# Kernel optimization log

Measured on AMD Instinct MI355X. Metric: run time of the kernel, lower is better.

## Reference

```python
import jax, jax.numpy as jnp
import numpy as np

B, S_NEW, D = 8, 16, 2048
H, HD = 16, 128
PAST = 4096


def setup_inputs() -> dict:
    key = jax.random.key(0)
    ks = jax.random.split(key, 8)
    w = 0.02
    return {
        "x": jax.random.normal(ks[0], (B, S_NEW, D), jnp.float32),
        "k_cache": jax.random.normal(ks[1], (B, H, PAST, HD), jnp.float32),
        "v_cache": jax.random.normal(ks[2], (B, H, PAST, HD), jnp.float32),
        "Wq": jax.random.normal(ks[3], (D, D), jnp.float32) * w,
        "bq": jnp.zeros((D,), jnp.float32),
        "Wk": jax.random.normal(ks[4], (D, D), jnp.float32) * w,
        "bk": jnp.zeros((D,), jnp.float32),
        "Wv": jax.random.normal(ks[5], (D, D), jnp.float32) * w,
        "bv": jnp.zeros((D,), jnp.float32),
        "Wo": jax.random.normal(ks[6], (D, D), jnp.float32) * w,
        "bo": jnp.zeros((D,), jnp.float32),
    }


def reference(x, k_cache, v_cache, Wq, bq, Wk, bk, Wv, bv, Wo, bo):
    B_, S_new, D_ = x.shape
    H_ = H
    hd = D_ // H_
    scale = hd ** (-0.5)

    def proj(W, b):
        # [B,S,D] -> [B,H,S,hd]
        return (x @ W + b).reshape(B_, S_new, H_, hd).transpose(0, 2, 1, 3)

    q = proj(Wq, bq)
    k_new = proj(Wk, bk)
    v_new = proj(Wv, bv)

    # cache.append + get_full_kv: concat along sequence axis
    k = jnp.concatenate([k_cache, k_new], axis=2)  # [B,H,S_full,hd]
    v = jnp.concatenate([v_cache, v_new], axis=2)
    S_full = k.shape[2]
    past = S_full - S_new

    scores = jnp.einsum("bhqd,bhkd->bhqk", q, k) * scale  # [B,H,S_new,S_full]

    # triu(ones(S_new,S_full), diagonal=past+1): mask key j when j - i > past
    i = jnp.arange(S_new)[:, None]
    j = jnp.arange(S_full)[None, :]
    mask = (j - i) > past  # [S_new, S_full] bool
    scores = jnp.where(mask[None, None, :, :], -jnp.inf, scores)

    attn = jax.nn.softmax(scores, axis=-1)  # dropout is identity in eval
    out = jnp.einsum("bhqk,bhkd->bhqd", attn, v)  # [B,H,S_new,hd]
    out = out.transpose(0, 2, 1, 3).reshape(B_, S_new, D_)
    return out @ Wo + bo
```

## Files before the change

### kernel.cpp

```cpp
#include <hip/hip_runtime.h>
#include <stdint.h>

#define B_    8
#define SNEW  16
#define D_    2048
#define H_    16
#define HD_   128
#define PAST_ 4096
#define SCALE 0.08838834764831845f

#define NCHUNK 16

typedef __attribute__((ext_vector_type(8))) short bf16x8;
typedef __attribute__((ext_vector_type(4))) float f32x4;

union BF8 { bf16x8 v; unsigned int u[4]; unsigned short s[8]; };

__device__ __forceinline__ unsigned short f2bf(float f) {
  union { float f; unsigned int u; } c; c.f = f;
  unsigned int r = c.u + 0x7fffu + ((c.u >> 16) & 1u);
  return (unsigned short)(r >> 16);
}
__device__ __forceinline__ unsigned int pk2(float a, float b) {
  return (unsigned int)f2bf(a) | ((unsigned int)f2bf(b) << 16);
}

__global__ __launch_bounds__(256) void k_cvt_x(const float* __restrict__ x,
                                               unsigned short* __restrict__ xb) {
  int i = blockIdx.x * 256 + threadIdx.x;
  const float4* xs = (const float4*)x;
  float4 a = xs[i * 2], b = xs[i * 2 + 1];
  uint4 v;
  v.x = pk2(a.x, a.y); v.y = pk2(a.z, a.w);
  v.z = pk2(b.x, b.y); v.w = pk2(b.z, b.w);
  ((uint4*)xb)[i] = v;
}

__global__ __launch_bounds__(256) void k_qkv(
    const unsigned short* __restrict__ xb,
    const float* __restrict__ Wq, const float* __restrict__ bq,
    const float* __restrict__ Wk, const float* __restrict__ bk,
    const float* __restrict__ Wv, const float* __restrict__ bv,
    unsigned short* __restrict__ qb, unsigned short* __restrict__ kbn,
    unsigned short* __restrict__ vbn) {
  __shared__ float red[4][128][16];
  const int n0g = blockIdx.x * 16;
  const int mat = n0g >> 11;
  const int n0 = n0g & 2047;
  const float* W    = (mat == 0) ? Wq : ((mat == 1) ? Wk : Wv);
  const float* bias = (mat == 0) ? bq : ((mat == 1) ? bk : bv);
  const int tid = threadIdx.x, w = tid >> 6, lane = tid & 63;
  const int nl = lane & 15, g = lane >> 4;

  f32x4 acc[8];
#pragma unroll
  for (int i = 0; i < 8; i++) acc[i] = (f32x4){0.f, 0.f, 0.f, 0.f};

  const int k0w = w * 512;
  for (int kc = 0; kc < 16; kc++) {
    const int kbase = k0w + kc * 32 + g * 8;
    float bw[8];
#pragma unroll
    for (int j = 0; j < 8; j++) bw[j] = W[(size_t)(kbase + j) * 2048 + n0 + nl];
    BF8 bf;
#pragma unroll
    for (int j2 = 0; j2 < 4; j2++) bf.u[j2] = pk2(bw[2 * j2], bw[2 * j2 + 1]);
#pragma unroll
    for (int mt = 0; mt < 8; mt++) {
      bf16x8 a = *(const bf16x8*)(xb + (size_t)(mt * 16 + nl) * 2048 + kbase);
      acc[mt] = __builtin_amdgcn_mfma_f32_16x16x32_bf16(a, bf.v, acc[mt], 0, 0, 0);
    }
  }
#pragma unroll
  for (int mt = 0; mt < 8; mt++) {
    red[w][mt * 16 + g * 4 + 0][nl] = acc[mt][0];
    red[w][mt * 16 + g * 4 + 1][nl] = acc[mt][1];
    red[w][mt * 16 + g * 4 + 2][nl] = acc[mt][2];
    red[w][mt * 16 + g * 4 + 3][nl] = acc[mt][3];
  }
  __syncthreads();
  const int m = tid >> 1;
  const int c0 = (tid & 1) * 8;
  float sv[8];
#pragma unroll
  for (int i = 0; i < 8; i++)
    sv[i] = red[0][m][c0 + i] + red[1][m][c0 + i] + red[2][m][c0 + i] +
            red[3][m][c0 + i] + bias[n0 + c0 + i];
  const int bb = m >> 4, srow = m & 15;
  const int nglob = n0 + c0;
  const int hh = nglob >> 7, dd = nglob & 127;
  size_t ob = (((size_t)(bb * H_ + hh) * SNEW + srow) * HD_ + dd);
  uint4 v;
  if (mat == 0) {
    v.x = pk2(sv[0] * SCALE, sv[1] * SCALE); v.y = pk2(sv[2] * SCALE, sv[3] * SCALE);
    v.z = pk2(sv[4] * SCALE, sv[5] * SCALE); v.w = pk2(sv[6] * SCALE, sv[7] * SCALE);
    *(uint4*)(qb + ob) = v;
  } else {
    v.x = pk2(sv[0], sv[1]); v.y = pk2(sv[2], sv[3]);
    v.z = pk2(sv[4], sv[5]); v.w = pk2(sv[6], sv[7]);
    if (mat == 1) *(uint4*)(kbn + ob) = v;
    else          *(uint4*)(vbn + ob) = v;
  }
}

__global__ __launch_bounds__(256) void k_attn(
    const float* __restrict__ kcache, const float* __restrict__ vcache,
    const unsigned short* __restrict__ qb, const unsigned short* __restrict__ kbn,
    const unsigned short* __restrict__ vbn,
    float* __restrict__ pO, float* __restrict__ pml) {
  __shared__ char smem[17408 * 2 + 4352 + 5120];
  unsigned short* Klds = (unsigned short*)smem;
  unsigned short* Vlds = (unsigned short*)(smem + 17408);
  unsigned short* Qlds = (unsigned short*)(smem + 34816);
  unsigned short* Plds = (unsigned short*)(smem + 34816 + 4352);
  float* cO  = (float*)smem;
  float* cml = (float*)(smem + 32768);

  const int chunk = blockIdx.x;
  const int h = blockIdx.y, b = blockIdx.z;
  const int bh = b * H_ + h;
  const int tid = threadIdx.x;
  const int w = tid >> 6, lane = tid & 63;
  const int nl = lane & 15, g = lane >> 4;

  {
    uint4 v = ((const uint4*)(qb + (size_t)bh * 2048))[tid];
    int e = tid * 8;
    *(uint4*)(Qlds + (e >> 7) * 136 + (e & 127)) = v;
  }
  for (int i = tid; i < 1280; i += 256) ((unsigned int*)Plds)[i] = 0u;
  __syncthreads();

  bf16x8 qfrag[4];
#pragma unroll
  for (int kc4 = 0; kc4 < 4; kc4++)
    qfrag[kc4] = *(const bf16x8*)(Qlds + nl * 136 + kc4 * 32 + g * 8);

  unsigned short* Kw = Klds + w * (16 * 136);
  unsigned short* Vw = Vlds + w * (16 * 136);
  unsigned short* Pw = Plds + w * (16 * 40);

  f32x4 Oacc[8];
#pragma unroll
  for (int i = 0; i < 8; i++) Oacc[i] = (f32x4){0.f, 0.f, 0.f, 0.f};
  float m_run = -1e30f, l_run = 0.f;

  const int CK = PAST_ / NCHUNK;
  const int key0 = chunk * CK + w * (CK / 4);
  const int NIT = CK / 4 / 16;
  const bool lastw = (chunk == NCHUNK - 1) && (w == 3);
  const int itend = NIT + (lastw ? 1 : 0);

  for (int it = 0; it < itend; it++) {
    if (it < NIT) {
      const float4* ks = (const float4*)(kcache + ((size_t)bh * PAST_ + key0 + it * 16) * HD_);
      const float4* vs = (const float4*)(vcache + ((size_t)bh * PAST_ + key0 + it * 16) * HD_);
#pragma unroll
      for (int i = 0; i < 8; i++) {
        float4 kv = ks[lane + i * 64];
        int e = (lane + i * 64) * 4;
        uint2 p; p.x = pk2(kv.x, kv.y); p.y = pk2(kv.z, kv.w);
        *(uint2*)(Kw + (e >> 7) * 136 + (e & 127)) = p;
      }
#pragma unroll
      for (int i = 0; i < 8; i++) {
        float4 vv = vs[lane + i * 64];
        int e = (lane + i * 64) * 4;
        uint2 p; p.x = pk2(vv.x, vv.y); p.y = pk2(vv.z, vv.w);
        *(uint2*)(Vw + (e >> 7) * 136 + (e & 127)) = p;
      }
    } else {
      const uint4* ks = (const uint4*)(kbn + (size_t)bh * 2048);
      const uint4* vs = (const uint4*)(vbn + (size_t)bh * 2048);
#pragma unroll
      for (int i = 0; i < 4; i++) {
        uint4 v = ks[lane + i * 64];
        int e = (lane + i * 64) * 8;
        *(uint4*)(Kw + (e >> 7) * 136 + (e & 127)) = v;
        uint4 v2 = vs[lane + i * 64];
        *(uint4*)(Vw + (e >> 7) * 136 + (e & 127)) = v2;
      }
    }

    f32x4 sacc = (f32x4){0.f, 0.f, 0.f, 0.f};
#pragma unroll
    for (int kc4 = 0; kc4 < 4; kc4++) {
      bf16x8 a = *(const bf16x8*)(Kw + nl * 136 + kc4 * 32 + g * 8);
      sacc = __builtin_amdgcn_mfma_f32_16x16x32_bf16(a, qfrag[kc4], sacc, 0, 0, 0);
    }
    float s0 = sacc[0], s1 = sacc[1], s2 = sacc[2], s3 = sacc[3];
    if (it == NIT) {
      if (g * 4 + 0 > nl) s0 = -1e30f;
      if (g * 4 + 1 > nl) s1 = -1e30f;
      if (g * 4 + 2 > nl) s2 = -1e30f;
      if (g * 4 + 3 > nl) s3 = -1e30f;
    }
    float kmax = fmaxf(fmaxf(s0, s1), fmaxf(s2, s3));
    kmax = fmaxf(kmax, __shfl_xor(kmax, 16, 64));
    kmax = fmaxf(kmax, __shfl_xor(kmax, 32, 64));
    float newm = fmaxf(m_run, kmax);
    float p0 = __expf(s0 - newm), p1 = __expf(s1 - newm);
    float p2 = __expf(s2 - newm), p3 = __expf(s3 - newm);
    float psum = p0 + p1 + p2 + p3;
    psum += __shfl_xor(psum, 16, 64);
    psum += __shfl_xor(psum, 32, 64);
    float alpha = __expf(m_run - newm);
    l_run = l_run * alpha + psum;
    m_run = newm;
    float ar0 = __shfl(alpha, g * 4 + 0, 64);
    float ar1 = __shfl(alpha, g * 4 + 1, 64);
    float ar2 = __shfl(alpha, g * 4 + 2, 64);
    float ar3 = __shfl(alpha, g * 4 + 3, 64);
#pragma unroll
    for (int nt = 0; nt < 8; nt++) {
      Oacc[nt][0] *= ar0; Oacc[nt][1] *= ar1;
      Oacc[nt][2] *= ar2; Oacc[nt][3] *= ar3;
    }
    *(unsigned int*)(Pw + nl * 40 + g * 4)     = pk2(p0, p1);
    *(unsigned int*)(Pw + nl * 40 + g * 4 + 2) = pk2(p2, p3);
    bf16x8 pfrag = *(const bf16x8*)(Pw + nl * 40 + g * 8);
#pragma unroll
    for (int nt = 0; nt < 8; nt++) {
      BF8 vb;
#pragma unroll
      for (int j2 = 0; j2 < 4; j2++) {
        int ka = (g * 8 + j2 * 2) & 15;
        int kb2 = (g * 8 + j2 * 2 + 1) & 15;
        unsigned int lo = Vw[ka * 136 + nt * 16 + nl];
        unsigned int hi = Vw[kb2 * 136 + nt * 16 + nl];
        vb.u[j2] = lo | (hi << 16);
      }
      Oacc[nt] = __builtin_amdgcn_mfma_f32_16x16x32_bf16(pfrag, vb.v, Oacc[nt], 0, 0, 0);
    }
  }

  __syncthreads();
  float* cOw = cO + w * (16 * 128);
#pragma unroll
  for (int nt = 0; nt < 8; nt++) {
    cOw[(g * 4 + 0) * 128 + nt * 16 + nl] = Oacc[nt][0];
    cOw[(g * 4 + 1) * 128 + nt * 16 + nl] = Oacc[nt][1];
    cOw[(g * 4 + 2) * 128 + nt * 16 + nl] = Oacc[nt][2];
    cOw[(g * 4 + 3) * 128 + nt * 16 + nl] = Oacc[nt][3];
  }
  if (g == 0) { cml[(w * 16 + nl) * 2] = m_run; cml[(w * 16 + nl) * 2 + 1] = l_run; }
  __syncthreads();

  const int q = tid >> 4;
  const int d0 = (tid & 15) * 8;
  float M = -1e30f, mws[4], lws[4];
#pragma unroll
  for (int ww = 0; ww < 4; ww++) {
    mws[ww] = cml[(ww * 16 + q) * 2];
    lws[ww] = cml[(ww * 16 + q) * 2 + 1];
    M = fmaxf(M, mws[ww]);
  }
  float L = 0.f, o[8];
#pragma unroll
  for (int i = 0; i < 8; i++) o[i] = 0.f;
#pragma unroll
  for (int ww = 0; ww < 4; ww++) {
    float Wt = __expf(mws[ww] - M);
    L += Wt * lws[ww];
    const float* src = cO + ww * 2048 + q * 128 + d0;
#pragma unroll
    for (int i = 0; i < 8; i++) o[i] += Wt * src[i];
  }
  size_t pb = (((size_t)bh * NCHUNK + chunk) * 16 + q) * 128 + d0;
  float4 st0 = {o[0], o[1], o[2], o[3]}, st1 = {o[4], o[5], o[6], o[7]};
  *(float4*)(pO + pb) = st0;
  *(float4*)(pO + pb + 4) = st1;
  if ((tid & 15) == 0) {
    size_t mb = (((size_t)bh * NCHUNK + chunk) * 16 + q) * 2;
    pml[mb] = M; pml[mb + 1] = L;
  }
}

__global__ __launch_bounds__(256) void k_comb(const float* __restrict__ pO,
                                              const float* __restrict__ pml,
                                              float* __restrict__ attn) {
  const int bh = blockIdx.x, tid = threadIdx.x;
  const int q = tid >> 4, d0 = (tid & 15) * 8;
  float M = -1e30f, mc[NCHUNK], lc[NCHUNK];
#pragma unroll
  for (int c = 0; c < NCHUNK; c++) {
    size_t mb = (((size_t)bh * NCHUNK + c) * 16 + q) * 2;
    mc[c] = pml[mb]; lc[c] = pml[mb + 1];
    M = fmaxf(M, mc[c]);
  }
  float L = 0.f, o[8];
#pragma unroll
  for (int i = 0; i < 8; i++) o[i] = 0.f;
#pragma unroll
  for (int c = 0; c < NCHUNK; c++) {
    float Wt = __expf(mc[c] - M);
    L += Wt * lc[c];
    const float* src = pO + (((size_t)bh * NCHUNK + c) * 16 + q) * 128 + d0;
#pragma unroll
    for (int i = 0; i < 8; i++) o[i] += Wt * src[i];
  }
  float inv = 1.f / L;
  int b = bh >> 4, h = bh & 15;
  float* dst = attn + ((size_t)(b * SNEW + q)) * D_ + h * HD_ + d0;
  float4 s0 = {o[0] * inv, o[1] * inv, o[2] * inv, o[3] * inv};
  float4 s1 = {o[4] * inv, o[5] * inv, o[6] * inv, o[7] * inv};
  *(float4*)dst = s0;
  *(float4*)(dst + 4) = s1;
}

__global__ __launch_bounds__(256) void k_oproj(const float* __restrict__ attn,
                                               const float* __restrict__ Wo,
                                               const float* __restrict__ bo,
                                               float* __restrict__ out) {
  __shared__ float red[4][128][16];
  const int n0 = blockIdx.x * 16;
  const int tid = threadIdx.x, w = tid >> 6, lane = tid & 63;
  const int nl = lane & 15, g = lane >> 4;
  f32x4 acc[8];
#pragma unroll
  for (int i = 0; i < 8; i++) acc[i] = (f32x4){0.f, 0.f, 0.f, 0.f};
  const int k0w = w * 512;
  for (int kc = 0; kc < 16; kc++) {
    const int kbase = k0w + kc * 32 + g * 8;
    float bw[8];
#pragma unroll
    for (int j = 0; j < 8; j++) bw[j] = Wo[(size_t)(kbase + j) * 2048 + n0 + nl];
    BF8 bf;
#pragma unroll
    for (int j2 = 0; j2 < 4; j2++) bf.u[j2] = pk2(bw[2 * j2], bw[2 * j2 + 1]);
#pragma unroll
    for (int mt = 0; mt < 8; mt++) {
      const float* ap = attn + (size_t)(mt * 16 + nl) * 2048 + kbase;
      float4 a0 = *(const float4*)ap;
      float4 a1 = *(const float4*)(ap + 4);
      BF8 af;
      af.u[0] = pk2(a0.x, a0.y); af.u[1] = pk2(a0.z, a0.w);
      af.u[2] = pk2(a1.x, a1.y); af.u[3] = pk2(a1.z, a1.w);
      acc[mt] = __builtin_amdgcn_mfma_f32_16x16x32_bf16(af.v, bf.v, acc[mt], 0, 0, 0);
    }
  }
#pragma unroll
  for (int mt = 0; mt < 8; mt++) {
    red[w][mt * 16 + g * 4 + 0][nl] = acc[mt][0];
    red[w][mt * 16 + g * 4 + 1][nl] = acc[mt][1];
    red[w][mt * 16 + g * 4 + 2][nl] = acc[mt][2];
    red[w][mt * 16 + g * 4 + 3][nl] = acc[mt][3];
  }
  __syncthreads();
  const int m = tid >> 1;
  const int c0 = (tid & 1) * 8;
  float sv[8];
#pragma unroll
  for (int i = 0; i < 8; i++)
    sv[i] = red[0][m][c0 + i] + red[1][m][c0 + i] + red[2][m][c0 + i] +
            red[3][m][c0 + i] + bo[n0 + c0 + i];
  float* dst = out + (size_t)m * 2048 + n0 + c0;
  float4 s0 = {sv[0], sv[1], sv[2], sv[3]}, s1 = {sv[4], sv[5], sv[6], sv[7]};
  *(float4*)dst = s0;
  *(float4*)(dst + 4) = s1;
}

extern "C" void kernel_launch(void* const* d_in, const int* in_sizes, int n_in,
                              void* d_out, int out_size, void* d_ws, size_t ws_size,
                              hipStream_t stream) {
  const float* x  = (const float*)d_in[0];
  const float* kc = (const float*)d_in[1];
  const float* vc = (const float*)d_in[2];
  const float* Wq = (const float*)d_in[3];
  const float* bq = (const float*)d_in[4];
  const float* Wk = (const float*)d_in[5];
  const float* bk = (const float*)d_in[6];
  const float* Wv = (const float*)d_in[7];
  const float* bv = (const float*)d_in[8];
  const float* Wo = (const float*)d_in[9];
  const float* bo = (const float*)d_in[10];
  float* out = (float*)d_out;

  char* ws = (char*)d_ws;
  unsigned short* xb   = (unsigned short*)(ws + 0);
  unsigned short* qb   = (unsigned short*)(ws + 524288);
  unsigned short* kbn  = (unsigned short*)(ws + 1048576);
  unsigned short* vbn  = (unsigned short*)(ws + 1572864);
  float*          attn = (float*)(ws + 2097152);
  float*          pO   = (float*)(ws + 3145728);
  float*          pml  = (float*)(ws + 19922944);

  k_cvt_x<<<128, 256, 0, stream>>>(x, xb);
  k_qkv<<<384, 256, 0, stream>>>(xb, Wq, bq, Wk, bk, Wv, bv, qb, kbn, vbn);
  k_attn<<<dim3(NCHUNK, H_, B_), 256, 0, stream>>>(kc, vc, qb, kbn, vbn, pO, pml);
  k_comb<<<B_ * H_, 256, 0, stream>>>(pO, pml, attn);
  k_oproj<<<128, 256, 0, stream>>>(attn, Wo, bo, out);
}
```

Before: 661.4 us.

## Prefetch K/V and weights into registers, transpose V in LDS, use exp2 softmax

The attention kernel now register-prefetches the next K/V cache tile while the current one is processed. V is stored transposed in LDS with an XOR swizzle so the PV MFMA operand loads become four dword reads instead of sixteen scattered shorts. Q is pre-scaled by log2(e) so the softmax can use exp2, and bf16 packing uses the hardware v_cvt_pk_bf16_f32 instruction. The projection GEMMs software-pipeline their weight loads one k-step ahead, and launch bounds request 3 blocks per SM, which adds register pressure and possible spills.

```diff
diff --git a/kernel.cpp b/kernel.cpp
--- a/kernel.cpp
+++ b/kernel.cpp
@@ -7,22 +7,24 @@
 #define H_    16
 #define HD_   128
 #define PAST_ 4096
+#define LOG2E 1.4426950408889634f
 #define SCALE 0.08838834764831845f
+#define QSCALE (SCALE * LOG2E)
 
 #define NCHUNK 16
+
+#define KSTRIDE 136
+#define VSTRIDE 18
 
 typedef __attribute__((ext_vector_type(8))) short bf16x8;
 typedef __attribute__((ext_vector_type(4))) float f32x4;
 
 union BF8 { bf16x8 v; unsigned int u[4]; unsigned short s[8]; };
 
-__device__ __forceinline__ unsigned short f2bf(float f) {
-  union { float f; unsigned int u; } c; c.f = f;
-  unsigned int r = c.u + 0x7fffu + ((c.u >> 16) & 1u);
-  return (unsigned short)(r >> 16);
-}
 __device__ __forceinline__ unsigned int pk2(float a, float b) {
-  return (unsigned int)f2bf(a) | ((unsigned int)f2bf(b) << 16);
+  unsigned int r;
+  asm("v_cvt_pk_bf16_f32 %0, %1, %2" : "=v"(r) : "v"(a), "v"(b));
+  return r;
 }
 
 __global__ __launch_bounds__(256) void k_cvt_x(const float* __restrict__ x,
@@ -57,11 +59,17 @@
   for (int i = 0; i < 8; i++) acc[i] = (f32x4){0.f, 0.f, 0.f, 0.f};
 
   const int k0w = w * 512;
+  float bw[8];
+#pragma unroll
+  for (int j = 0; j < 8; j++) bw[j] = W[(size_t)(k0w + g * 8 + j) * 2048 + n0 + nl];
+
   for (int kc = 0; kc < 16; kc++) {
     const int kbase = k0w + kc * 32 + g * 8;
-    float bw[8];
-#pragma unroll
-    for (int j = 0; j < 8; j++) bw[j] = W[(size_t)(kbase + j) * 2048 + n0 + nl];
+    float nbw[8];
+    if (kc < 15) {
+#pragma unroll
+      for (int j = 0; j < 8; j++) nbw[j] = W[(size_t)(kbase + 32 + j) * 2048 + n0 + nl];
+    }
     BF8 bf;
 #pragma unroll
     for (int j2 = 0; j2 < 4; j2++) bf.u[j2] = pk2(bw[2 * j2], bw[2 * j2 + 1]);
@@ -69,6 +77,10 @@
     for (int mt = 0; mt < 8; mt++) {
       bf16x8 a = *(const bf16x8*)(xb + (size_t)(mt * 16 + nl) * 2048 + kbase);
       acc[mt] = __builtin_amdgcn_mfma_f32_16x16x32_bf16(a, bf.v, acc[mt], 0, 0, 0);
+    }
+    if (kc < 15) {
+#pragma unroll
+      for (int j = 0; j < 8; j++) bw[j] = nbw[j];
     }
   }
 #pragma unroll
@@ -92,8 +104,8 @@
   size_t ob = (((size_t)(bb * H_ + hh) * SNEW + srow) * HD_ + dd);
   uint4 v;
   if (mat == 0) {
-    v.x = pk2(sv[0] * SCALE, sv[1] * SCALE); v.y = pk2(sv[2] * SCALE, sv[3] * SCALE);
-    v.z = pk2(sv[4] * SCALE, sv[5] * SCALE); v.w = pk2(sv[6] * SCALE, sv[7] * SCALE);
+    v.x = pk2(sv[0] * QSCALE, sv[1] * QSCALE); v.y = pk2(sv[2] * QSCALE, sv[3] * QSCALE);
+    v.z = pk2(sv[4] * QSCALE, sv[5] * QSCALE); v.w = pk2(sv[6] * QSCALE, sv[7] * QSCALE);
     *(uint4*)(qb + ob) = v;
   } else {
     v.x = pk2(sv[0], sv[1]); v.y = pk2(sv[2], sv[3]);
@@ -103,16 +115,15 @@
   }
 }
 
-__global__ __launch_bounds__(256) void k_attn(
+__global__ __launch_bounds__(256, 3) void k_attn(
     const float* __restrict__ kcache, const float* __restrict__ vcache,
     const unsigned short* __restrict__ qb, const unsigned short* __restrict__ kbn,
     const unsigned short* __restrict__ vbn,
     float* __restrict__ pO, float* __restrict__ pml) {
-  __shared__ char smem[17408 * 2 + 4352 + 5120];
+  __shared__ char smem[40960];
   unsigned short* Klds = (unsigned short*)smem;
   unsigned short* Vlds = (unsigned short*)(smem + 17408);
-  unsigned short* Qlds = (unsigned short*)(smem + 34816);
-  unsigned short* Plds = (unsigned short*)(smem + 34816 + 4352);
+  unsigned short* QP   = (unsigned short*)(smem + 35840);
   float* cO  = (float*)smem;
   float* cml = (float*)(smem + 32768);
 
@@ -123,51 +134,74 @@
   const int w = tid >> 6, lane = tid & 63;
   const int nl = lane & 15, g = lane >> 4;
 
-  {
-    uint4 v = ((const uint4*)(qb + (size_t)bh * 2048))[tid];
-    int e = tid * 8;
-    *(uint4*)(Qlds + (e >> 7) * 136 + (e & 127)) = v;
-  }
-  for (int i = tid; i < 1280; i += 256) ((unsigned int*)Plds)[i] = 0u;
-  __syncthreads();
-
-  bf16x8 qfrag[4];
-#pragma unroll
-  for (int kc4 = 0; kc4 < 4; kc4++)
-    qfrag[kc4] = *(const bf16x8*)(Qlds + nl * 136 + kc4 * 32 + g * 8);
-
-  unsigned short* Kw = Klds + w * (16 * 136);
-  unsigned short* Vw = Vlds + w * (16 * 136);
-  unsigned short* Pw = Plds + w * (16 * 40);
-
-  f32x4 Oacc[8];
-#pragma unroll
-  for (int i = 0; i < 8; i++) Oacc[i] = (f32x4){0.f, 0.f, 0.f, 0.f};
-  float m_run = -1e30f, l_run = 0.f;
-
   const int CK = PAST_ / NCHUNK;
   const int key0 = chunk * CK + w * (CK / 4);
   const int NIT = CK / 4 / 16;
   const bool lastw = (chunk == NCHUNK - 1) && (w == 3);
   const int itend = NIT + (lastw ? 1 : 0);
 
+  const float4* kbase = (const float4*)(kcache + ((size_t)bh * PAST_ + key0) * HD_);
+  const float4* vbase = (const float4*)(vcache + ((size_t)bh * PAST_ + key0) * HD_);
+
+  float4 kreg[8], vreg[8];
+#pragma unroll
+  for (int i = 0; i < 8; i++) kreg[i] = kbase[lane + i * 64];
+#pragma unroll
+  for (int i = 0; i < 8; i++) vreg[i] = vbase[lane + i * 64];
+
+  {
+    uint4 v = ((const uint4*)(qb + (size_t)bh * 2048))[tid];
+    int e = tid * 8;
+    *(uint4*)(QP + (e >> 7) * KSTRIDE + (e & 127)) = v;
+  }
+  __syncthreads();
+  bf16x8 qfrag[4];
+#pragma unroll
+  for (int kc4 = 0; kc4 < 4; kc4++)
+    qfrag[kc4] = *(const bf16x8*)(QP + nl * KSTRIDE + kc4 * 32 + g * 8);
+  __syncthreads();
+  for (int i = tid; i < 1280; i += 256) ((unsigned int*)QP)[i] = 0u;
+  __syncthreads();
+
+  unsigned short* Kw = Klds + w * (16 * KSTRIDE);
+  unsigned short* Vw = Vlds + w * (128 * VSTRIDE);
+  unsigned short* Pw = QP + w * (16 * 40);
+
+  f32x4 Oacc[8];
+#pragma unroll
+  for (int i = 0; i < 8; i++) Oacc[i] = (f32x4){0.f, 0.f, 0.f, 0.f};
+  float m_run = -1e30f, l_run = 0.f;
+
   for (int it = 0; it < itend; it++) {
     if (it < NIT) {
-      const float4* ks = (const float4*)(kcache + ((size_t)bh * PAST_ + key0 + it * 16) * HD_);
-      const float4* vs = (const float4*)(vcache + ((size_t)bh * PAST_ + key0 + it * 16) * HD_);
 #pragma unroll
       for (int i = 0; i < 8; i++) {
-        float4 kv = ks[lane + i * 64];
+        float4 kv = kreg[i];
         int e = (lane + i * 64) * 4;
         uint2 p; p.x = pk2(kv.x, kv.y); p.y = pk2(kv.z, kv.w);
-        *(uint2*)(Kw + (e >> 7) * 136 + (e & 127)) = p;
+        *(uint2*)(Kw + (e >> 7) * KSTRIDE + (e & 127)) = p;
       }
 #pragma unroll
       for (int i = 0; i < 8; i++) {
-        float4 vv = vs[lane + i * 64];
-        int e = (lane + i * 64) * 4;
-        uint2 p; p.x = pk2(vv.x, vv.y); p.y = pk2(vv.z, vv.w);
-        *(uint2*)(Vw + (e >> 7) * 136 + (e & 127)) = p;
+        float4 vv = vreg[i];
+        int idx = lane + i * 64;
+        int r = idx >> 5;
+        int d0 = (idx & 31) * 4;
+        unsigned int c01 = pk2(vv.x, vv.y);
+        unsigned int c23 = pk2(vv.z, vv.w);
+        int rs = r ^ (((d0 >> 5) & 1) << 3);
+        Vw[(d0 + 0) * VSTRIDE + rs] = (unsigned short)c01;
+        Vw[(d0 + 1) * VSTRIDE + rs] = (unsigned short)(c01 >> 16);
+        Vw[(d0 + 2) * VSTRIDE + rs] = (unsigned short)c23;
+        Vw[(d0 + 3) * VSTRIDE + rs] = (unsigned short)(c23 >> 16);
+      }
+      if (it + 1 < NIT) {
+        const float4* kn = kbase + (size_t)(it + 1) * 512;
+        const float4* vn = vbase + (size_t)(it + 1) * 512;
+#pragma unroll
+        for (int i = 0; i < 8; i++) kreg[i] = kn[lane + i * 64];
+#pragma unroll
+        for (int i = 0; i < 8; i++) vreg[i] = vn[lane + i * 64];
       }
     } else {
       const uint4* ks = (const uint4*)(kbn + (size_t)bh * 2048);
@@ -176,16 +210,28 @@
       for (int i = 0; i < 4; i++) {
         uint4 v = ks[lane + i * 64];
         int e = (lane + i * 64) * 8;
-        *(uint4*)(Kw + (e >> 7) * 136 + (e & 127)) = v;
+        *(uint4*)(Kw + (e >> 7) * KSTRIDE + (e & 127)) = v;
+      }
+#pragma unroll
+      for (int i = 0; i < 4; i++) {
         uint4 v2 = vs[lane + i * 64];
-        *(uint4*)(Vw + (e >> 7) * 136 + (e & 127)) = v2;
+        int idx = lane + i * 64;
+        int r = idx >> 4;
+        int d0 = (idx & 15) * 8;
+        int rs = r ^ (((d0 >> 5) & 1) << 3);
+        unsigned int uu[4] = {v2.x, v2.y, v2.z, v2.w};
+#pragma unroll
+        for (int j2 = 0; j2 < 4; j2++) {
+          Vw[(d0 + 2 * j2 + 0) * VSTRIDE + rs] = (unsigned short)uu[j2];
+          Vw[(d0 + 2 * j2 + 1) * VSTRIDE + rs] = (unsigned short)(uu[j2] >> 16);
+        }
       }
     }
 
     f32x4 sacc = (f32x4){0.f, 0.f, 0.f, 0.f};
 #pragma unroll
     for (int kc4 = 0; kc4 < 4; kc4++) {
-      bf16x8 a = *(const bf16x8*)(Kw + nl * 136 + kc4 * 32 + g * 8);
+      bf16x8 a = *(const bf16x8*)(Kw + nl * KSTRIDE + kc4 * 32 + g * 8);
       sacc = __builtin_amdgcn_mfma_f32_16x16x32_bf16(a, qfrag[kc4], sacc, 0, 0, 0);
     }
     float s0 = sacc[0], s1 = sacc[1], s2 = sacc[2], s3 = sacc[3];
@@ -199,12 +245,12 @@
     kmax = fmaxf(kmax, __shfl_xor(kmax, 16, 64));
     kmax = fmaxf(kmax, __shfl_xor(kmax, 32, 64));
     float newm = fmaxf(m_run, kmax);
-    float p0 = __expf(s0 - newm), p1 = __expf(s1 - newm);
-    float p2 = __expf(s2 - newm), p3 = __expf(s3 - newm);
+    float p0 = exp2f(s0 - newm), p1 = exp2f(s1 - newm);
+    float p2 = exp2f(s2 - newm), p3 = exp2f(s3 - newm);
     float psum = p0 + p1 + p2 + p3;
     psum += __shfl_xor(psum, 16, 64);
     psum += __shfl_xor(psum, 32, 64);
-    float alpha = __expf(m_run - newm);
+    float alpha = exp2f(m_run - newm);
     l_run = l_run * alpha + psum;
     m_run = newm;
     float ar0 = __shfl(alpha, g * 4 + 0, 64);
@@ -221,15 +267,11 @@
     bf16x8 pfrag = *(const bf16x8*)(Pw + nl * 40 + g * 8);
 #pragma unroll
     for (int nt = 0; nt < 8; nt++) {
+      int row = nt * 16 + nl;
+      const unsigned int* vp = (const unsigned int*)(
+          Vw + row * VSTRIDE + (((g & 1) << 3) ^ ((nt & 2) << 2)));
       BF8 vb;
-#pragma unroll
-      for (int j2 = 0; j2 < 4; j2++) {
-        int ka = (g * 8 + j2 * 2) & 15;
-        int kb2 = (g * 8 + j2 * 2 + 1) & 15;
-        unsigned int lo = Vw[ka * 136 + nt * 16 + nl];
-        unsigned int hi = Vw[kb2 * 136 + nt * 16 + nl];
-        vb.u[j2] = lo | (hi << 16);
-      }
+      vb.u[0] = vp[0]; vb.u[1] = vp[1]; vb.u[2] = vp[2]; vb.u[3] = vp[3];
       Oacc[nt] = __builtin_amdgcn_mfma_f32_16x16x32_bf16(pfrag, vb.v, Oacc[nt], 0, 0, 0);
     }
   }
@@ -260,7 +302,7 @@
   for (int i = 0; i < 8; i++) o[i] = 0.f;
 #pragma unroll
   for (int ww = 0; ww < 4; ww++) {
-    float Wt = __expf(mws[ww] - M);
+    float Wt = exp2f(mws[ww] - M);
     L += Wt * lws[ww];
     const float* src = cO + ww * 2048 + q * 128 + d0;
 #pragma unroll
@@ -293,7 +335,7 @@
   for (int i = 0; i < 8; i++) o[i] = 0.f;
 #pragma unroll
   for (int c = 0; c < NCHUNK; c++) {
-    float Wt = __expf(mc[c] - M);
+    float Wt = exp2f(mc[c] - M);
     L += Wt * lc[c];
     const float* src = pO + (((size_t)bh * NCHUNK + c) * 16 + q) * 128 + d0;
 #pragma unroll
@@ -320,11 +362,16 @@
 #pragma unroll
   for (int i = 0; i < 8; i++) acc[i] = (f32x4){0.f, 0.f, 0.f, 0.f};
   const int k0w = w * 512;
+  float bw[8];
+#pragma unroll
+  for (int j = 0; j < 8; j++) bw[j] = Wo[(size_t)(k0w + g * 8 + j) * 2048 + n0 + nl];
   for (int kc = 0; kc < 16; kc++) {
     const int kbase = k0w + kc * 32 + g * 8;
-    float bw[8];
-#pragma unroll
-    for (int j = 0; j < 8; j++) bw[j] = Wo[(size_t)(kbase + j) * 2048 + n0 + nl];
+    float nbw[8];
+    if (kc < 15) {
+#pragma unroll
+      for (int j = 0; j < 8; j++) nbw[j] = Wo[(size_t)(kbase + 32 + j) * 2048 + n0 + nl];
+    }
     BF8 bf;
 #pragma unroll
     for (int j2 = 0; j2 < 4; j2++) bf.u[j2] = pk2(bw[2 * j2], bw[2 * j2 + 1]);
@@ -337,6 +384,10 @@
       af.u[0] = pk2(a0.x, a0.y); af.u[1] = pk2(a0.z, a0.w);
       af.u[2] = pk2(a1.x, a1.y); af.u[3] = pk2(a1.z, a1.w);
       acc[mt] = __builtin_amdgcn_mfma_f32_16x16x32_bf16(af.v, bf.v, acc[mt], 0, 0, 0);
+    }
+    if (kc < 15) {
+#pragma unroll
+      for (int j = 0; j < 8; j++) bw[j] = nbw[j];
     }
   }
 #pragma unroll
```

Measured after the change: 665.6 us. Within noise of the previous version (+0.6%).
